# Optimization experiments

Measured on AMD Instinct MI355X. Metric: run time of the kernel, lower is better.

Reference implementation:

```python
import jax, jax.numpy as jnp
import numpy as np

TWO_PI = 2.0 * np.pi

def _round_ste(y):
    # forward: round(y); backward: identity (straight-through), matching _RoundSTE
    return y + jax.lax.stop_gradient(jnp.round(y) - y)

def _anti_wrap(x):
    return jnp.abs(x - _round_ste(x / TWO_PI) * TWO_PI)

def setup_inputs() -> dict:
    key = jax.random.key(0)
    k1, k2 = jax.random.split(key)
    B, F, T = 32, 513, 1600  # F = n_fft//2 + 1 with n_fft=1024
    phase_r = jax.random.normal(k1, (B, F, T), dtype=jnp.float32)
    phase_g = jax.random.normal(k2, (B, F, T), dtype=jnp.float32)
    return {"phase_r": phase_r, "phase_g": phase_g}

def reference(phase_r, phase_g):
    # d[b,f,t] = phase_r - phase_g
    d = phase_r - phase_g
    ip_loss = jnp.mean(_anti_wrap(d))

    # GD_matrix has -1 on diag, +1 on superdiag; matmul(phase^T, M)[b,t,f]
    # = phase[b,f-1,t] - phase[b,f,t] (with implicit zero at f=-1).
    # GD_r - GD_g is the same banded diff applied to d along freq axis.
    d_shift_f = jnp.pad(d, ((0, 0), (1, 0), (0, 0)))[:, :-1, :]  # d[b,f-1,t], 0 at f=0
    gd_loss = jnp.mean(_anti_wrap(d_shift_f - d))

    # PTD_matrix: same banded diff along time axis.
    d_shift_t = jnp.pad(d, ((0, 0), (0, 0), (1, 0)))[:, :, :-1]  # d[b,f,t-1], 0 at t=0
    ptd_loss = jnp.mean(_anti_wrap(d_shift_t - d))

    return (ip_loss, gd_loss, ptd_loss)
```

## Files before the change

### kernel.cpp

```cpp
#include <hip/hip_runtime.h>
#include <math.h>

constexpr int Bc = 32, Fc = 513, Tc = 1600;
constexpr int FCH = 8;
constexpr int SPB = 65;
constexpr int NSTRIP = Bc * SPB;
constexpr int WPB = 4;
constexpr int BLK = 64 * WPB;
constexpr int NBLK = NSTRIP / WPB;
constexpr long long NTOT = (long long)Bc * Fc * Tc;

typedef float f32x2 __attribute__((ext_vector_type(2)));

__device__ __forceinline__ f32x2 pk_fma(f32x2 a, f32x2 b, f32x2 c) {
    f32x2 d;
    asm("v_pk_fma_f32 %0, %1, %2, %3" : "=v"(d) : "v"(a), "v"(b), "v"(c));
    return d;
}
__device__ __forceinline__ f32x2 pk_add(f32x2 a, f32x2 b) {
    f32x2 d;
    asm("v_pk_add_f32 %0, %1, %2" : "=v"(d) : "v"(a), "v"(b));
    return d;
}
__device__ __forceinline__ f32x2 pk_mul(f32x2 a, f32x2 b) {
    f32x2 d;
    asm("v_pk_mul_f32 %0, %1, %2" : "=v"(d) : "v"(a), "v"(b));
    return d;
}

#define INV2PI 0.15915494309189535f
#define MAGICF 12582912.0f
#define N2PI  -6.283185307179586f

__device__ __forceinline__ void aw_acc(f32x2 x, float& sA, float& sB,
                                       f32x2 cinv, f32x2 cmag, f32x2 cnmag,
                                       f32x2 cn2pi) {
    f32x2 y = pk_fma(x, cinv, cmag);
    f32x2 r = pk_add(y, cnmag);
    f32x2 w = pk_fma(r, cn2pi, x);
    sA += fabsf(w.x);
    sB += fabsf(w.y);
}

__global__ __launch_bounds__(BLK) void phase_main(
        const float* __restrict__ pr, const float* __restrict__ pg,
        float* __restrict__ partials,
        float* __restrict__ out,
        int use_atomic)
{
    const int lane = (int)threadIdx.x & 63;
    const int wv   = (int)blockIdx.x * WPB + ((int)threadIdx.x >> 6);
    const int b    = wv / SPB;
    const int k    = wv - b * SPB;
    const int f0   = k * FCH;
    const int len  = (k == SPB - 1) ? 1 : FCH;

    const size_t rowbase = ((size_t)b * Fc + (size_t)f0) * Tc;
    const float* ap = pr + rowbase;
    const float* gp = pg + rowbase;

    const f32x2 cneg1 = {-1.0f, -1.0f};
    const f32x2 cinv  = {INV2PI, INV2PI};
    const f32x2 cmag  = {MAGICF, MAGICF};
    const f32x2 cnmag = {-MAGICF, -MAGICF};
    const f32x2 cn2pi = {N2PI, N2PI};
    const float mtail = (lane < 16) ? 1.0f : 0.0f;
    const f32x2 m2    = {mtail, mtail};

    float ipA = 0.f, ipB = 0.f, gdA = 0.f, gdB = 0.f, ptA = 0.f, ptB = 0.f;

    float4 A[7], G[7], Dc[7], Dp[7];

    auto load_row = [&](const float* p, float4* R) {
        #pragma unroll
        for (int c = 0; c < 6; ++c)
            R[c] = *(const float4*)(p + c * 256 + lane * 4);
        if (lane < 16) R[6] = *(const float4*)(p + 1536 + lane * 4);
        else           R[6] = make_float4(0.f, 0.f, 0.f, 0.f);
    };
    auto diff7 = [&](float4* D, const float4* X, const float4* Y) {
        #pragma unroll
        for (int c = 0; c < 7; ++c) {
            f32x2 x01 = {X[c].x, X[c].y}, x23 = {X[c].z, X[c].w};
            f32x2 y01 = {Y[c].x, Y[c].y}, y23 = {Y[c].z, Y[c].w};
            f32x2 d01 = pk_fma(y01, cneg1, x01);
            f32x2 d23 = pk_fma(y23, cneg1, x23);
            D[c] = make_float4(d01.x, d01.y, d23.x, d23.y);
        }
    };
    auto acc_row = [&](const float4* D, const float4* P) {
        #pragma unroll
        for (int c = 0; c < 7; ++c) {
            f32x2 d01 = {D[c].x, D[c].y}, d23 = {D[c].z, D[c].w};
            f32x2 p01 = {P[c].x, P[c].y}, p23 = {P[c].z, P[c].w};
            float up    = __shfl_up(D[c].w, 1);
            float carry = (c == 0) ? 0.f : __shfl(D[c - 1].w, 63);
            float dm1   = (lane == 0) ? carry : up;
            f32x2 sh01 = {dm1, D[c].x};
            f32x2 sh23 = {D[c].y, D[c].z};
            f32x2 pdd01 = pk_fma(d01, cneg1, p01);
            f32x2 pdd23 = pk_fma(d23, cneg1, p23);
            f32x2 tdd01 = pk_fma(d01, cneg1, sh01);
            f32x2 tdd23 = pk_fma(d23, cneg1, sh23);
            if (c == 6) {
                tdd01 = pk_mul(tdd01, m2);
                tdd23 = pk_mul(tdd23, m2);
            }
            aw_acc(d01,  ipA, ipB, cinv, cmag, cnmag, cn2pi);
            aw_acc(d23,  ipA, ipB, cinv, cmag, cnmag, cn2pi);
            aw_acc(pdd01, gdA, gdB, cinv, cmag, cnmag, cn2pi);
            aw_acc(pdd23, gdA, gdB, cinv, cmag, cnmag, cn2pi);
            aw_acc(tdd01, ptA, ptB, cinv, cmag, cnmag, cn2pi);
            aw_acc(tdd23, ptA, ptB, cinv, cmag, cnmag, cn2pi);
        }
    };

    load_row(ap, A);
    load_row(gp, G);
    if (f0 > 0) {
        float4 Pa[7], Pg[7];
        load_row(ap - Tc, Pa);
        load_row(gp - Tc, Pg);
        diff7(Dp, Pa, Pg);
    } else {
        #pragma unroll
        for (int c = 0; c < 7; ++c) Dp[c] = make_float4(0.f, 0.f, 0.f, 0.f);
    }
    diff7(Dc, A, G);

    if (len == 1) {
        acc_row(Dc, Dp);
    } else {
        for (int i = 0; i < FCH; i += 2) {
            const size_t o1 = (size_t)min(i + 1, FCH - 1) * Tc;
            load_row(ap + o1, A);
            load_row(gp + o1, G);
            acc_row(Dc, Dp);
            diff7(Dp, A, G);
            const size_t o2 = (size_t)min(i + 2, FCH - 1) * Tc;
            load_row(ap + o2, A);
            load_row(gp + o2, G);
            acc_row(Dp, Dc);
            diff7(Dc, A, G);
        }
    }

    float s_ip = ipA + ipB, s_gd = gdA + gdB, s_ptd = ptA + ptB;
    #pragma unroll
    for (int off = 32; off > 0; off >>= 1) {
        s_ip  += __shfl_down(s_ip, off);
        s_gd  += __shfl_down(s_gd, off);
        s_ptd += __shfl_down(s_ptd, off);
    }
    __shared__ float sm[3][WPB];
    const int wid = (int)threadIdx.x >> 6;
    if (lane == 0) { sm[0][wid] = s_ip; sm[1][wid] = s_gd; sm[2][wid] = s_ptd; }
    __syncthreads();
    if (threadIdx.x == 0) {
        float a = 0.f, bb = 0.f, c = 0.f;
        #pragma unroll
        for (int w = 0; w < WPB; ++w) { a += sm[0][w]; bb += sm[1][w]; c += sm[2][w]; }
        if (use_atomic) {
            const float invN = (float)(1.0 / (double)NTOT);
            atomicAdd(out + 0, a * invN);
            atomicAdd(out + 1, bb * invN);
            atomicAdd(out + 2, c * invN);
        } else {
            partials[0 * NBLK + blockIdx.x] = a;
            partials[1 * NBLK + blockIdx.x] = bb;
            partials[2 * NBLK + blockIdx.x] = c;
        }
    }
}

__global__ __launch_bounds__(256) void phase_reduce(
        const float* __restrict__ partials, float* __restrict__ out)
{
    const int c = blockIdx.x;
    const int tid = threadIdx.x;
    float s = 0.f;
    for (int i = tid; i < NBLK; i += 256) s += partials[(size_t)c * NBLK + i];
    #pragma unroll
    for (int off = 32; off > 0; off >>= 1) s += __shfl_down(s, off);
    __shared__ float sm[4];
    const int lane = tid & 63, wid = tid >> 6;
    if (lane == 0) sm[wid] = s;
    __syncthreads();
    if (tid == 0) {
        float t = sm[0] + sm[1] + sm[2] + sm[3];
        out[c] = t * (float)(1.0 / (double)NTOT);
    }
}

__global__ void zero3(float* out) {
    if (threadIdx.x < 3) out[threadIdx.x] = 0.f;
}

extern "C" void kernel_launch(void* const* d_in, const int* in_sizes, int n_in,
                              void* d_out, int out_size, void* d_ws, size_t ws_size,
                              hipStream_t stream) {
    const float* pr = (const float*)d_in[0];
    const float* pg = (const float*)d_in[1];
    float* out = (float*)d_out;

    if (ws_size >= (size_t)NBLK * 3 * sizeof(float)) {
        float* partials = (float*)d_ws;
        phase_main<<<NBLK, BLK, 0, stream>>>(pr, pg, partials, nullptr, 0);
        phase_reduce<<<3, 256, 0, stream>>>(partials, out);
    } else {
        zero3<<<1, 64, 0, stream>>>(out);
        phase_main<<<NBLK, BLK, 0, stream>>>(pr, pg, nullptr, out, 1);
    }
}
```

Baseline: 48.01 us.

## Use one-wave blocks, longer frequency strips, and last-block-done final reduction

Each block is now a single 64-lane wave, and it covers 16 frequency rows instead of 8, so there are 33 strips per batch and 1056 blocks instead of 520 blocks of four waves. The separate reduce kernel is removed. Each wave writes its partial sums, bumps an atomic counter, and the last wave to finish sums all partials, which saves a kernel launch. The cost is an extra memset on the stream, fewer waves in flight, and a serial final reduction done by one wave.

```diff
diff --git a/kernel.cpp b/kernel.cpp
--- a/kernel.cpp
+++ b/kernel.cpp
@@ -2,12 +2,9 @@
 #include <math.h>
 
 constexpr int Bc = 32, Fc = 513, Tc = 1600;
-constexpr int FCH = 8;
-constexpr int SPB = 65;
-constexpr int NSTRIP = Bc * SPB;
-constexpr int WPB = 4;
-constexpr int BLK = 64 * WPB;
-constexpr int NBLK = NSTRIP / WPB;
+constexpr int FCH = 16;
+constexpr int SPB = 33;
+constexpr int NBLK = Bc * SPB;
 constexpr long long NTOT = (long long)Bc * Fc * Tc;
 
 typedef float f32x2 __attribute__((ext_vector_type(2)));
@@ -42,14 +39,15 @@
     sB += fabsf(w.y);
 }
 
-__global__ __launch_bounds__(BLK) void phase_main(
+__global__ __launch_bounds__(64) void phase_main(
         const float* __restrict__ pr, const float* __restrict__ pg,
         float* __restrict__ partials,
+        unsigned* __restrict__ counter,
         float* __restrict__ out,
         int use_atomic)
 {
-    const int lane = (int)threadIdx.x & 63;
-    const int wv   = (int)blockIdx.x * WPB + ((int)threadIdx.x >> 6);
+    const int lane = (int)threadIdx.x;
+    const int wv   = (int)blockIdx.x;
     const int b    = wv / SPB;
     const int k    = wv - b * SPB;
     const int f0   = k * FCH;
@@ -152,43 +150,44 @@
         s_gd  += __shfl_down(s_gd, off);
         s_ptd += __shfl_down(s_ptd, off);
     }
-    __shared__ float sm[3][WPB];
-    const int wid = (int)threadIdx.x >> 6;
-    if (lane == 0) { sm[0][wid] = s_ip; sm[1][wid] = s_gd; sm[2][wid] = s_ptd; }
-    __syncthreads();
-    if (threadIdx.x == 0) {
-        float a = 0.f, bb = 0.f, c = 0.f;
-        #pragma unroll
-        for (int w = 0; w < WPB; ++w) { a += sm[0][w]; bb += sm[1][w]; c += sm[2][w]; }
-        if (use_atomic) {
+
+    if (use_atomic) {
+        if (lane == 0) {
             const float invN = (float)(1.0 / (double)NTOT);
-            atomicAdd(out + 0, a * invN);
-            atomicAdd(out + 1, bb * invN);
-            atomicAdd(out + 2, c * invN);
-        } else {
-            partials[0 * NBLK + blockIdx.x] = a;
-            partials[1 * NBLK + blockIdx.x] = bb;
-            partials[2 * NBLK + blockIdx.x] = c;
-        }
-    }
-}
-
-__global__ __launch_bounds__(256) void phase_reduce(
-        const float* __restrict__ partials, float* __restrict__ out)
-{
-    const int c = blockIdx.x;
-    const int tid = threadIdx.x;
-    float s = 0.f;
-    for (int i = tid; i < NBLK; i += 256) s += partials[(size_t)c * NBLK + i];
-    #pragma unroll
-    for (int off = 32; off > 0; off >>= 1) s += __shfl_down(s, off);
-    __shared__ float sm[4];
-    const int lane = tid & 63, wid = tid >> 6;
-    if (lane == 0) sm[wid] = s;
-    __syncthreads();
-    if (tid == 0) {
-        float t = sm[0] + sm[1] + sm[2] + sm[3];
-        out[c] = t * (float)(1.0 / (double)NTOT);
+            atomicAdd(out + 0, s_ip * invN);
+            atomicAdd(out + 1, s_gd * invN);
+            atomicAdd(out + 2, s_ptd * invN);
+        }
+        return;
+    }
+
+    if (lane == 0) {
+        partials[0 * NBLK + wv] = s_ip;
+        partials[1 * NBLK + wv] = s_gd;
+        partials[2 * NBLK + wv] = s_ptd;
+    }
+    int last = 0;
+    if (lane == 0) {
+        __threadfence();
+        unsigned old = __hip_atomic_fetch_add(counter, 1u, __ATOMIC_ACQ_REL,
+                                              __HIP_MEMORY_SCOPE_AGENT);
+        last = (old == (unsigned)(NBLK - 1));
+    }
+    last = __shfl(last, 0);
+    if (last) {
+        const float invN = (float)(1.0 / (double)NTOT);
+        #pragma unroll
+        for (int c = 0; c < 3; ++c) {
+            float s = 0.f;
+            for (int i = lane; i < NBLK; i += 64)
+                s += __hip_atomic_load(&partials[c * NBLK + i],
+                                       __ATOMIC_RELAXED,
+                                       __HIP_MEMORY_SCOPE_AGENT);
+            #pragma unroll
+            for (int off = 32; off > 0; off >>= 1)
+                s += __shfl_down(s, off);
+            if (lane == 0) out[c] = s * invN;
+        }
     }
 }
 
@@ -203,12 +202,15 @@
     const float* pg = (const float*)d_in[1];
     float* out = (float*)d_out;
 
-    if (ws_size >= (size_t)NBLK * 3 * sizeof(float)) {
+    const size_t need = (size_t)NBLK * 3 * sizeof(float) + sizeof(unsigned);
+    if (ws_size >= need) {
         float* partials = (float*)d_ws;
-        phase_main<<<NBLK, BLK, 0, stream>>>(pr, pg, partials, nullptr, 0);
-        phase_reduce<<<3, 256, 0, stream>>>(partials, out);
+        unsigned* counter = (unsigned*)((char*)d_ws
+                          + (size_t)NBLK * 3 * sizeof(float));
+        hipMemsetAsync(counter, 0, sizeof(unsigned), stream);
+        phase_main<<<NBLK, 64, 0, stream>>>(pr, pg, partials, counter, out, 0);
     } else {
         zero3<<<1, 64, 0, stream>>>(out);
-        phase_main<<<NBLK, BLK, 0, stream>>>(pr, pg, nullptr, out, 1);
-    }
-}
+        phase_main<<<NBLK, 64, 0, stream>>>(pr, pg, nullptr, nullptr, out, 1);
+    }
+}
```

Measured after the change: 92.78 us. 93.3% more time.
